# Optimization experiments

Measured on AMD Instinct MI355X. Metric: run time of the kernel, lower is better.

## Reference

```python
import jax, jax.numpy as jnp
import numpy as np

LAYERS, STACKS = 10, 4
DILATIONS = [2 ** l for _ in range(STACKS) for l in range(LAYERS)]  # 40 blocks


def setup_inputs() -> dict:
    key = jax.random.key(0)
    ks = jax.random.split(key, 7)
    B, C, L, SC, NB = 4, 64, 8192, 256, len(DILATIONS)
    scale = 0.05  # keep 40 stacked residual blocks numerically tame
    return {
        "x": jax.random.normal(ks[0], (B, C, L), dtype=jnp.float32),
        "dc_w": jax.random.normal(ks[1], (NB, C, C, 2), dtype=jnp.float32) * scale,
        "dc_b": jax.random.normal(ks[2], (NB, C), dtype=jnp.float32) * scale,
        "conv_w": jax.random.normal(ks[3], (NB, C, C), dtype=jnp.float32) * scale,
        "conv_b": jax.random.normal(ks[4], (NB, C), dtype=jnp.float32) * scale,
        "skip_w": jax.random.normal(ks[5], (NB, SC, C), dtype=jnp.float32) * scale,
        "skip_b": jax.random.normal(ks[6], (NB, SC), dtype=jnp.float32) * scale,
        "skip_size": 4096,
    }


def reference(x, dc_w, dc_b, conv_w, conv_b, skip_w, skip_b, skip_size):
    # x: [B, res_ch, L]; returns stacked skips [n_blocks, B, skip_ch, skip_size]
    out = x
    skips = []
    for i, d in enumerate(DILATIONS):
        h = (jnp.einsum('oi,bil->bol', dc_w[i, :, :, 0], out[:, :, :-d])
             + jnp.einsum('oi,bil->bol', dc_w[i, :, :, 1], out[:, :, d:])
             + dc_b[i][None, :, None])
        g = jax.nn.relu(h)
        r = jnp.einsum('oi,bil->bol', conv_w[i], g) + conv_b[i][None, :, None]
        out = r + out[:, :, -r.shape[2]:]  # residual on aligned (last) timesteps
        s = jnp.einsum('oi,bil->bol', skip_w[i], g) + skip_b[i][None, :, None]
        skips.append(s[:, :, -skip_size:])
    return jnp.stack(skips)
```

## Files before the change

### kernel.cpp

```cpp
#include <hip/hip_runtime.h>


#define CC    64
#define SCC   256
#define BB    4
#define LL0   8192
#define NBLK  40
#define SKIPN 4096

typedef __attribute__((ext_vector_type(8))) short bf16x8;
typedef __attribute__((ext_vector_type(4))) float f32x4;
typedef unsigned short us;

__device__ __forceinline__ us f2bf(float f) {
    union { float f; unsigned u; } v; v.f = f;
    return (us)((v.u + 0x7FFF + ((v.u >> 16) & 1)) >> 16);
}
__device__ __forceinline__ unsigned pk2(float a, float b) {
    return (unsigned)f2bf(a) | ((unsigned)f2bf(b) << 16);
}
__device__ __forceinline__ uint2 pk4(f32x4 v) {
    return (uint2){pk2(v[0], v[1]), pk2(v[2], v[3])};
}
__device__ __forceinline__ bf16x8 pack8(f32x4 u0, f32x4 u1) {
    bf16x8 r;
    r[0]=(short)f2bf(u0[0]); r[1]=(short)f2bf(u0[1]);
    r[2]=(short)f2bf(u0[2]); r[3]=(short)f2bf(u0[3]);
    r[4]=(short)f2bf(u1[0]); r[5]=(short)f2bf(u1[1]);
    r[6]=(short)f2bf(u1[2]); r[7]=(short)f2bf(u1[3]);
    return r;
}
__device__ __forceinline__ int sws(int r, int c) {
    return (r << 6) + ((((c >> 3) ^ r) & 7) << 3) + (c & 7);
}
__device__ __forceinline__ int scb(int s, int chunk) {
    return (s << 6) + (((chunk ^ (s & 7)) & 7) << 3);
}

__global__ __launch_bounds__(256) void prep_kernel(
    const float* __restrict__ x, float* __restrict__ xt_out,
    const float* __restrict__ dc_w, const float* __restrict__ conv_w,
    const float* __restrict__ skip_w,
    us* __restrict__ wcat, us* __restrict__ cwb, us* __restrict__ swb)
{
    if (blockIdx.x < 512) {
        __shared__ float tile[64][65];
        const int b = blockIdx.x >> 7, t0 = (blockIdx.x & 127) * 64;
        const int tid = threadIdx.x;
        #pragma unroll
        for (int p = 0; p < 4; ++p) {
            const int c = p * 16 + (tid >> 4), j = tid & 15;
            const float4 v = *(const float4*)(x + ((size_t)b * CC + c) * LL0 + t0 + j * 4);
            tile[c][j*4+0]=v.x; tile[c][j*4+1]=v.y; tile[c][j*4+2]=v.z; tile[c][j*4+3]=v.w;
        }
        __syncthreads();
        #pragma unroll
        for (int p = 0; p < 4; ++p) {
            const int r = p * 16 + (tid >> 4), h = tid & 15;
            float4 v = {tile[h*4+0][r], tile[h*4+1][r], tile[h*4+2][r], tile[h*4+3][r]};
            *(float4*)(xt_out + ((size_t)b * LL0 + t0 + r) * CC + h * 4) = v;
        }
        return;
    }
    const int n_sw = NBLK * SCC * CC, n_cw = NBLK * CC * CC, n_wc = NBLK * CC * 128;
    for (int idx = (blockIdx.x - 512) * blockDim.x + threadIdx.x; idx < n_sw;
         idx += 1024 * blockDim.x) {
        swb[idx] = f2bf(skip_w[idx]);
        if (idx < n_cw) cwb[idx] = f2bf(conv_w[idx]);
        if (idx < n_wc) {
            const int i = idx >> 13, o = (idx >> 7) & 63, kk = idx & 127;
            wcat[idx] = f2bf(dc_w[(((i * CC + o) * CC) + (kk & 63)) * 2 + (kk >> 6)]);
        }
    }
}

template<int NW>
__device__ __forceinline__ void skip_body(
    int e, int blk0,
    const us* __restrict__ g_all, const us* __restrict__ swb,
    const float* __restrict__ skip_b, float* __restrict__ out)
{
    constexpr int ROWS = NW * 16;
    constexpr int TPB = (SKIPN / ROWS) * BB;
    const int tid = threadIdx.x, lane = tid & 63, wv = tid >> 6;
    const int j = blk0 + e / TPB;
    const int id = e % TPB;
    const int tt = id % (SKIPN / ROWS);
    const int b  = id / (SKIPN / ROWS);
    const us* g  = g_all + ((size_t)j * BB + b) * SKIPN * CC;
    const us* sw = swb + (size_t)j * SCC * CC;
    const float* sb = skip_b + j * SCC;
    float* op = out + ((size_t)j * BB + b) * SCC * SKIPN;

    const int trow = tt * ROWS + wv * 16 + (lane & 15);
    bf16x8 a[2];
    a[0] = *(const bf16x8*)(g + (size_t)trow * CC + (lane >> 4) * 8);
    a[1] = *(const bf16x8*)(g + (size_t)trow * CC + 32 + (lane >> 4) * 8);
    const int tstore = tt * ROWS + wv * 16 + ((lane >> 4) << 2);
    #pragma unroll 4
    for (int n = 0; n < 16; ++n) {
        const int sc = n * 16 + (lane & 15);
        const float bias = sb[sc];
        f32x4 acc = (f32x4){bias, bias, bias, bias};
        const us* wrow = sw + sc * CC + (lane >> 4) * 8;
        acc = __builtin_amdgcn_mfma_f32_16x16x32_bf16(a[0], *(const bf16x8*)(wrow), acc, 0, 0, 0);
        acc = __builtin_amdgcn_mfma_f32_16x16x32_bf16(a[1], *(const bf16x8*)(wrow + 32), acc, 0, 0, 0);
        *(float4*)(op + (size_t)sc * SKIPN + tstore) = (float4){acc[0], acc[1], acc[2], acc[3]};
    }
}

__global__ __launch_bounds__(512) void fused6_kernel(
    const float* __restrict__ cur, float* __restrict__ nxt,
    const us* __restrict__ wcat_all, const us* __restrict__ cwb_all,
    const float* __restrict__ db_all, const float* __restrict__ cb_all,
    us* __restrict__ g_all, int blk0, int Lin, int ntiles,
    const us* __restrict__ swb, const float* __restrict__ skip_b,
    float* __restrict__ out, int pb0)
{
    const int wg = blockIdx.x, chain = BB * ntiles;
    if (wg >= chain) { skip_body<8>(wg - chain, pb0, g_all, swb, skip_b, out); return; }

    constexpr int TOUT = 96, R0 = 159, RCAP = 160;
    __shared__ __align__(16) float sm[RCAP * CC];
    __shared__ __align__(16) us  scr[8 * 16 * CC];

    const int tid = threadIdx.x, lane = tid & 63, wv = tid >> 6;
    const int b = wg / ntiles, t0 = (wg % ntiles) * TOUT;
    const float* src = cur + (size_t)b * LL0 * CC;
    const int s = lane & 15, q = lane >> 4;
    us* myscr = scr + wv * (16 * CC);

    for (int base = 0; base < R0; base += 32) {
        const int row = base + (tid >> 4);
        const int h4 = (tid & 15) * 4;
        if (row < R0) {
            int gt = t0 + row; if (gt > Lin - 1) gt = Lin - 1;
            *(f32x4*)(sm + sws(row, h4)) = *(const f32x4*)(src + (size_t)gt * CC + h4);
        }
    }
    __syncthreads();

    int Rcur = R0, Lj = Lin;
    for (int j = 0; j < 6; ++j) {
        const int d = 1 << j;
        const int Rn = Rcur - d;
        Lj -= d;
        const us* wj = wcat_all + (size_t)(blk0 + j) * CC * 128;
        const us* cj = cwb_all + (size_t)(blk0 + j) * CC * CC;
        const float* dbj = db_all + (blk0 + j) * CC;
        const float* cbj = cb_all + (blk0 + j) * CC;
        const int wbase = Lj - SKIPN;
        us* gdst = g_all + ((size_t)(blk0 + j) * BB + b) * SKIPN * CC;

        f32x4 r2[2][4];
        #pragma unroll
        for (int fi = 0; fi < 2; ++fi) {
            const int fg = wv + fi * 8;
            const bool act = fg * 16 < Rn;
            if (act) {
                const int t = fg * 16 + s;
                const int tc = t > Rn - 1 ? Rn - 1 : t;
                bf16x8 af0 = pack8(*(const f32x4*)(sm + sws(tc, q * 8)),
                                   *(const f32x4*)(sm + sws(tc, q * 8 + 4)));
                bf16x8 af1 = pack8(*(const f32x4*)(sm + sws(tc, 32 + q * 8)),
                                   *(const f32x4*)(sm + sws(tc, 36 + q * 8)));
                bf16x8 af2 = pack8(*(const f32x4*)(sm + sws(tc + d, q * 8)),
                                   *(const f32x4*)(sm + sws(tc + d, q * 8 + 4)));
                bf16x8 af3 = pack8(*(const f32x4*)(sm + sws(tc + d, 32 + q * 8)),
                                   *(const f32x4*)(sm + sws(tc + d, 36 + q * 8)));
                #pragma unroll
                for (int n = 0; n < 4; ++n) {
                    const int o0 = n * 16 + q * 4;
                    f32x4 acc = *(const f32x4*)(dbj + o0);
                    const us* wr = wj + (n * 16 + s) * 128 + q * 8;
                    acc = __builtin_amdgcn_mfma_f32_16x16x32_bf16(*(const bf16x8*)(wr),      af0, acc, 0, 0, 0);
                    acc = __builtin_amdgcn_mfma_f32_16x16x32_bf16(*(const bf16x8*)(wr + 32), af1, acc, 0, 0, 0);
                    acc = __builtin_amdgcn_mfma_f32_16x16x32_bf16(*(const bf16x8*)(wr + 64), af2, acc, 0, 0, 0);
                    acc = __builtin_amdgcn_mfma_f32_16x16x32_bf16(*(const bf16x8*)(wr + 96), af3, acc, 0, 0, 0);
                    #pragma unroll
                    for (int r = 0; r < 4; ++r) acc[r] = acc[r] > 0.f ? acc[r] : 0.f;
                    *(uint2*)(myscr + scb(s, n * 2 + (q >> 1)) + (q & 1) * 4) = pk4(acc);
                }
                {
                    const int gt = t0 + t;
                    if (t < Rn && gt >= wbase && gt < Lj) {
                        us* gr = gdst + (size_t)(gt - wbase) * CC;
                        #pragma unroll
                        for (int h = 0; h < 2; ++h) {
                            const int ck = q * 2 + h;
                            *(bf16x8*)(gr + ck * 8) = *(const bf16x8*)(myscr + scb(s, ck));
                        }
                    }
                }
                bf16x8 g0 = *(const bf16x8*)(myscr + scb(s, q));
                bf16x8 g1 = *(const bf16x8*)(myscr + scb(s, 4 + q));
                #pragma unroll
                for (int n = 0; n < 4; ++n) {
                    const int o0 = n * 16 + q * 4;
                    f32x4 r = *(const f32x4*)(cbj + o0);
                    const us* wr = cj + (n * 16 + s) * CC + q * 8;
                    r = __builtin_amdgcn_mfma_f32_16x16x32_bf16(*(const bf16x8*)(wr),      g0, r, 0, 0, 0);
                    r = __builtin_amdgcn_mfma_f32_16x16x32_bf16(*(const bf16x8*)(wr + 32), g1, r, 0, 0, 0);
                    r += *(const f32x4*)(sm + sws(tc + d, o0));
                    r2[fi][n] = r;
                }
            }
        }
        __syncthreads();
        #pragma unroll
        for (int fi = 0; fi < 2; ++fi) {
            const int fg = wv + fi * 8;
            const int t = fg * 16 + s;
            if (t < Rn) {
                #pragma unroll
                for (int n = 0; n < 4; ++n)
                    *(f32x4*)(sm + sws(t, n * 16 + q * 4)) = r2[fi][n];
            }
        }
        __syncthreads();
        Rcur = Rn;
    }

    float* dst = nxt + (size_t)b * LL0 * CC;
    for (int base = 0; base < TOUT; base += 32) {
        const int row = base + (tid >> 4);
        const int h4 = (tid & 15) * 4;
        const int gt = t0 + row;
        if (row < TOUT && gt < Lj)
            *(float4*)(dst + (size_t)gt * CC + h4) = *(const float4*)(sm + sws(row, h4));
    }
}

template<int D>
__global__ __launch_bounds__(256) void pair_kernel(
    const float* __restrict__ cur, float* __restrict__ nxt,
    const us* __restrict__ wA, const us* __restrict__ wB,
    const us* __restrict__ cA, const us* __restrict__ cB,
    const float* __restrict__ dbA, const float* __restrict__ dbB,
    const float* __restrict__ cbA, const float* __restrict__ cbB,
    us* __restrict__ gA_out, us* __restrict__ gB_out,
    int Lin, int ntB,
    const us* __restrict__ g_all, const us* __restrict__ swb,
    const float* __restrict__ skip_b, float* __restrict__ out, int pb0)
{
    const int wg = blockIdx.x, chain = BB * ntB;
    if (wg >= chain) { skip_body<4>(wg - chain, pb0, g_all, swb, skip_b, out); return; }

    __shared__ __align__(16) float xs[4 * 32 * CC];
    __shared__ __align__(16) float ms[2 * 32 * CC];
    __shared__ __align__(16) us  scr[4 * 16 * CC];

    const int tid = threadIdx.x, lane = tid & 63, wv = tid >> 6;
    const int b = wg / ntB, T0 = (wg % ntB) * 32;
    const float* src = cur + (size_t)b * LL0 * CC;
    const int s = lane & 15, q = lane >> 4;
    us* myscr = scr + wv * (16 * CC);
    const int LoutA = Lin - D, Lout2 = Lin - 3 * D;

    #pragma unroll
    for (int p = 0; p < 8; ++p) {
        const int row = p * 16 + (tid >> 4);
        const int st = row >> 5, r = row & 31;
        const int h4 = (tid & 15) * 4;
        int gt = T0 + st * D + r; if (gt > Lin - 1) gt = Lin - 1;
        *(f32x4*)(xs + st * (32 * CC) + sws(r, h4)) =
            *(const f32x4*)(src + (size_t)gt * CC + h4);
    }
    __syncthreads();

    {
        const int m = wv >> 1, rA = (wv & 1) * 16 + s;
        const int tA = T0 + m * 2 * D + rA;
        const float* x0 = xs + (2 * m) * (32 * CC);
        const float* x1 = xs + (2 * m + 1) * (32 * CC);
        bf16x8 af0 = pack8(*(const f32x4*)(x0 + sws(rA, q * 8)),
                           *(const f32x4*)(x0 + sws(rA, q * 8 + 4)));
        bf16x8 af1 = pack8(*(const f32x4*)(x0 + sws(rA, 32 + q * 8)),
                           *(const f32x4*)(x0 + sws(rA, 36 + q * 8)));
        bf16x8 af2 = pack8(*(const f32x4*)(x1 + sws(rA, q * 8)),
                           *(const f32x4*)(x1 + sws(rA, q * 8 + 4)));
        bf16x8 af3 = pack8(*(const f32x4*)(x1 + sws(rA, 32 + q * 8)),
                           *(const f32x4*)(x1 + sws(rA, 36 + q * 8)));
        #pragma unroll
        for (int n = 0; n < 4; ++n) {
            const int o0 = n * 16 + q * 4;
            f32x4 acc = *(const f32x4*)(dbA + o0);
            const us* wr = wA + (n * 16 + s) * 128 + q * 8;
            acc = __builtin_amdgcn_mfma_f32_16x16x32_bf16(*(const bf16x8*)(wr),      af0, acc, 0, 0, 0);
            acc = __builtin_amdgcn_mfma_f32_16x16x32_bf16(*(const bf16x8*)(wr + 32), af1, acc, 0, 0, 0);
            acc = __builtin_amdgcn_mfma_f32_16x16x32_bf16(*(const bf16x8*)(wr + 64), af2, acc, 0, 0, 0);
            acc = __builtin_amdgcn_mfma_f32_16x16x32_bf16(*(const bf16x8*)(wr + 96), af3, acc, 0, 0, 0);
            #pragma unroll
            for (int r = 0; r < 4; ++r) acc[r] = acc[r] > 0.f ? acc[r] : 0.f;
            *(uint2*)(myscr + scb(s, n * 2 + (q >> 1)) + (q & 1) * 4) = pk4(acc);
        }
        {
            const int wbA = LoutA - SKIPN;
            const bool own = (m == 0) || (tA >= ntB * 32);
            if (own && tA >= wbA && tA < LoutA) {
                us* gr = gA_out + ((size_t)b * SKIPN + (tA - wbA)) * CC;
                #pragma unroll
                for (int h = 0; h < 2; ++h) {
                    const int ck = q * 2 + h;
                    *(bf16x8*)(gr + ck * 8) = *(const bf16x8*)(myscr + scb(s, ck));
                }
            }
        }
        bf16x8 g0 = *(const bf16x8*)(myscr + scb(s, q));
        bf16x8 g1 = *(const bf16x8*)(myscr + scb(s, 4 + q));
        #pragma unroll
        for (int n = 0; n < 4; ++n) {
            const int o0 = n * 16 + q * 4;
            f32x4 r = *(const f32x4*)(cbA + o0);
            const us* wr = cA + (n * 16 + s) * CC + q * 8;
            r = __builtin_amdgcn_mfma_f32_16x16x32_bf16(*(const bf16x8*)(wr),      g0, r, 0, 0, 0);
            r = __builtin_amdgcn_mfma_f32_16x16x32_bf16(*(const bf16x8*)(wr + 32), g1, r, 0, 0, 0);
            r += *(const f32x4*)(x1 + sws(rA, o0));
            *(f32x4*)(ms + m * (32 * CC) + sws(rA, o0)) = r;
        }
    }
    __syncthreads();

    {
        const int rB = (wv & 1) * 16 + s;
        const int tB = T0 + rB;
        const bool lead = wv < 2;
        const float* m0 = ms;
        const float* m1 = ms + 32 * CC;
        bf16x8 af0 = pack8(*(const f32x4*)(m0 + sws(rB, q * 8)),
                           *(const f32x4*)(m0 + sws(rB, q * 8 + 4)));
        bf16x8 af1 = pack8(*(const f32x4*)(m0 + sws(rB, 32 + q * 8)),
                           *(const f32x4*)(m0 + sws(rB, 36 + q * 8)));
        bf16x8 af2 = pack8(*(const f32x4*)(m1 + sws(rB, q * 8)),
                           *(const f32x4*)(m1 + sws(rB, q * 8 + 4)));
        bf16x8 af3 = pack8(*(const f32x4*)(m1 + sws(rB, 32 + q * 8)),
                           *(const f32x4*)(m1 + sws(rB, 36 + q * 8)));
        #pragma unroll
        for (int n = 0; n < 4; ++n) {
            const int o0 = n * 16 + q * 4;
            f32x4 acc = *(const f32x4*)(dbB + o0);
            const us* wr = wB + (n * 16 + s) * 128 + q * 8;
            acc = __builtin_amdgcn_mfma_f32_16x16x32_bf16(*(const bf16x8*)(wr),      af0, acc, 0, 0, 0);
            acc = __builtin_amdgcn_mfma_f32_16x16x32_bf16(*(const bf16x8*)(wr + 32), af1, acc, 0, 0, 0);
            acc = __builtin_amdgcn_mfma_f32_16x16x32_bf16(*(const bf16x8*)(wr + 64), af2, acc, 0, 0, 0);
            acc = __builtin_amdgcn_mfma_f32_16x16x32_bf16(*(const bf16x8*)(wr + 96), af3, acc, 0, 0, 0);
            #pragma unroll
            for (int r = 0; r < 4; ++r) acc[r] = acc[r] > 0.f ? acc[r] : 0.f;
            *(uint2*)(myscr + scb(s, n * 2 + (q >> 1)) + (q & 1) * 4) = pk4(acc);
        }
        {
            const int wbB = Lout2 - SKIPN;
            if (lead && tB >= wbB && tB < Lout2) {
                us* gr = gB_out + ((size_t)b * SKIPN + (tB - wbB)) * CC;
                #pragma unroll
                for (int h = 0; h < 2; ++h) {
                    const int ck = q * 2 + h;
                    *(bf16x8*)(gr + ck * 8) = *(const bf16x8*)(myscr + scb(s, ck));
                }
            }
        }
        bf16x8 g0 = *(const bf16x8*)(myscr + scb(s, q));
        bf16x8 g1 = *(const bf16x8*)(myscr + scb(s, 4 + q));
        float* dst = nxt + (size_t)b * LL0 * CC;
        #pragma unroll
        for (int n = 0; n < 4; ++n) {
            const int o0 = n * 16 + q * 4;
            f32x4 r = *(const f32x4*)(cbB + o0);
            const us* wr = cB + (n * 16 + s) * CC + q * 8;
            r = __builtin_amdgcn_mfma_f32_16x16x32_bf16(*(const bf16x8*)(wr),      g0, r, 0, 0, 0);
            r = __builtin_amdgcn_mfma_f32_16x16x32_bf16(*(const bf16x8*)(wr + 32), g1, r, 0, 0, 0);
            r += *(const f32x4*)(m1 + sws(rB, o0));
            if (lead && tB < Lout2)
                *(f32x4*)(dst + (size_t)tB * CC + o0) = r;
        }
    }
}

__global__ __launch_bounds__(256) void skip_kernel(
    const us* __restrict__ g_all, const us* __restrict__ swb,
    const float* __restrict__ skip_b, float* __restrict__ out, int blk0)
{
    skip_body<4>(blockIdx.x, blk0, g_all, swb, skip_b, out);
}

extern "C" void kernel_launch(void* const* d_in, const int* in_sizes, int n_in,
                              void* d_out, int out_size, void* d_ws, size_t ws_size,
                              hipStream_t stream)
{
    const float* x      = (const float*)d_in[0];
    const float* dc_w   = (const float*)d_in[1];
    const float* dc_b   = (const float*)d_in[2];
    const float* conv_w = (const float*)d_in[3];
    const float* conv_b = (const float*)d_in[4];
    const float* skip_w = (const float*)d_in[5];
    const float* skip_b = (const float*)d_in[6];
    float* out = (float*)d_out;

    char* ws = (char*)d_ws;
    float* bufA = (float*)ws;  ws += (size_t)BB * LL0 * CC * 4;
    float* bufB = (float*)ws;  ws += (size_t)BB * LL0 * CC * 4;
    us* g_all = (us*)ws;       ws += (size_t)NBLK * BB * SKIPN * CC * 2;
    us* wcat  = (us*)ws;       ws += (size_t)NBLK * CC * 128 * 2;
    us* cwb   = (us*)ws;       ws += (size_t)NBLK * CC * CC * 2;
    us* swb   = (us*)ws;       ws += (size_t)NBLK * SCC * CC * 2;

    prep_kernel<<<1536, 256, 0, stream>>>(x, bufA, dc_w, conv_w, skip_w, wcat, cwb, swb);

    float* bufs[2] = {bufA, bufB};
    const size_t GSZ = (size_t)BB * SKIPN * CC;
    int Lc = LL0, blk = 0, q = 0, produced = 0, skipped = 0;
    for (int st = 0; st < 4; ++st) {
        {
            const int Lout = Lc - 63;
            const int nt = (Lout + 95) / 96;
            int cap = produced - skipped; if (cap > 4) cap = 4;
            fused6_kernel<<<dim3(BB * nt + cap * 128), 512, 0, stream>>>(
                bufs[q & 1], bufs[(q + 1) & 1], wcat, cwb, dc_b, conv_b,
                g_all, blk, Lc, nt, swb, skip_b, out, skipped);
            skipped += cap; produced += 6; blk += 6; Lc = Lout; ++q;
        }
        #pragma unroll
        for (int pi = 0; pi < 2; ++pi) {
            const int D = pi == 0 ? 64 : 256;
            const int Lout2 = Lc - 3 * D;
            const int nt = (Lout2 + 31) / 32;
            int cap = produced - skipped; if (cap > 4) cap = 4;
            const int grid = BB * nt + cap * 256;
            if (D == 64)
                pair_kernel<64><<<dim3(grid), 256, 0, stream>>>(
                    bufs[q & 1], bufs[(q + 1) & 1],
                    wcat + (size_t)blk * CC * 128, wcat + (size_t)(blk + 1) * CC * 128,
                    cwb + (size_t)blk * CC * CC, cwb + (size_t)(blk + 1) * CC * CC,
                    dc_b + blk * CC, dc_b + (blk + 1) * CC,
                    conv_b + blk * CC, conv_b + (blk + 1) * CC,
                    g_all + (size_t)blk * GSZ, g_all + (size_t)(blk + 1) * GSZ,
                    Lc, nt, g_all, swb, skip_b, out, skipped);
            else
                pair_kernel<256><<<dim3(grid), 256, 0, stream>>>(
                    bufs[q & 1], bufs[(q + 1) & 1],
                    wcat + (size_t)blk * CC * 128, wcat + (size_t)(blk + 1) * CC * 128,
                    cwb + (size_t)blk * CC * CC, cwb + (size_t)(blk + 1) * CC * CC,
                    dc_b + blk * CC, dc_b + (blk + 1) * CC,
                    conv_b + blk * CC, conv_b + (blk + 1) * CC,
                    g_all + (size_t)blk * GSZ, g_all + (size_t)(blk + 1) * GSZ,
                    Lc, nt, g_all, swb, skip_b, out, skipped);
            skipped += cap; produced += 2; blk += 2; Lc = Lout2; ++q;
        }
    }
    const int rem = NBLK - skipped;
    if (rem > 0)
        skip_kernel<<<dim3(rem * 256), 256, 0, stream>>>(g_all, swb, skip_b, out, skipped);
}
```

Measured before the change: 770.5 us.

## Move skip GEMMs into one final kernel and keep bf16 shadow copy in fused6

Skip-projection work is no longer piggybacked as extra workgroups inside the fused6 and pair chain kernels. All 40 blocks' skip outputs are now computed by a single skip_all_kernel launched at the end. Separately, fused6 keeps a bf16 copy of the residual tile in shared memory, so the MFMA A-operands are loaded directly instead of being converted from fp32 on every read. This gives up the overlap of skip writes with the sequential chain and adds shared memory and extra stores in exchange for less conversion work and simpler chain kernels.

```diff
diff --git a/kernel.cpp b/kernel.cpp
--- a/kernel.cpp
+++ b/kernel.cpp
@@ -22,15 +22,10 @@
 __device__ __forceinline__ uint2 pk4(f32x4 v) {
     return (uint2){pk2(v[0], v[1]), pk2(v[2], v[3])};
 }
-__device__ __forceinline__ bf16x8 pack8(f32x4 u0, f32x4 u1) {
-    bf16x8 r;
-    r[0]=(short)f2bf(u0[0]); r[1]=(short)f2bf(u0[1]);
-    r[2]=(short)f2bf(u0[2]); r[3]=(short)f2bf(u0[3]);
-    r[4]=(short)f2bf(u1[0]); r[5]=(short)f2bf(u1[1]);
-    r[6]=(short)f2bf(u1[2]); r[7]=(short)f2bf(u1[3]);
-    return r;
-}
 __device__ __forceinline__ int sws(int r, int c) {
+    return (r << 6) + ((((c >> 3) ^ r) & 7) << 3) + (c & 7);
+}
+__device__ __forceinline__ int swh(int r, int c) {
     return (r << 6) + ((((c >> 3) ^ r) & 7) << 3) + (c & 7);
 }
 __device__ __forceinline__ int scb(int s, int chunk) {
@@ -74,58 +69,19 @@
     }
 }
 
-template<int NW>
-__device__ __forceinline__ void skip_body(
-    int e, int blk0,
-    const us* __restrict__ g_all, const us* __restrict__ swb,
-    const float* __restrict__ skip_b, float* __restrict__ out)
-{
-    constexpr int ROWS = NW * 16;
-    constexpr int TPB = (SKIPN / ROWS) * BB;
-    const int tid = threadIdx.x, lane = tid & 63, wv = tid >> 6;
-    const int j = blk0 + e / TPB;
-    const int id = e % TPB;
-    const int tt = id % (SKIPN / ROWS);
-    const int b  = id / (SKIPN / ROWS);
-    const us* g  = g_all + ((size_t)j * BB + b) * SKIPN * CC;
-    const us* sw = swb + (size_t)j * SCC * CC;
-    const float* sb = skip_b + j * SCC;
-    float* op = out + ((size_t)j * BB + b) * SCC * SKIPN;
-
-    const int trow = tt * ROWS + wv * 16 + (lane & 15);
-    bf16x8 a[2];
-    a[0] = *(const bf16x8*)(g + (size_t)trow * CC + (lane >> 4) * 8);
-    a[1] = *(const bf16x8*)(g + (size_t)trow * CC + 32 + (lane >> 4) * 8);
-    const int tstore = tt * ROWS + wv * 16 + ((lane >> 4) << 2);
-    #pragma unroll 4
-    for (int n = 0; n < 16; ++n) {
-        const int sc = n * 16 + (lane & 15);
-        const float bias = sb[sc];
-        f32x4 acc = (f32x4){bias, bias, bias, bias};
-        const us* wrow = sw + sc * CC + (lane >> 4) * 8;
-        acc = __builtin_amdgcn_mfma_f32_16x16x32_bf16(a[0], *(const bf16x8*)(wrow), acc, 0, 0, 0);
-        acc = __builtin_amdgcn_mfma_f32_16x16x32_bf16(a[1], *(const bf16x8*)(wrow + 32), acc, 0, 0, 0);
-        *(float4*)(op + (size_t)sc * SKIPN + tstore) = (float4){acc[0], acc[1], acc[2], acc[3]};
-    }
-}
-
 __global__ __launch_bounds__(512) void fused6_kernel(
     const float* __restrict__ cur, float* __restrict__ nxt,
     const us* __restrict__ wcat_all, const us* __restrict__ cwb_all,
     const float* __restrict__ db_all, const float* __restrict__ cb_all,
-    us* __restrict__ g_all, int blk0, int Lin, int ntiles,
-    const us* __restrict__ swb, const float* __restrict__ skip_b,
-    float* __restrict__ out, int pb0)
+    us* __restrict__ g_all, int blk0, int Lin, int ntiles)
 {
-    const int wg = blockIdx.x, chain = BB * ntiles;
-    if (wg >= chain) { skip_body<8>(wg - chain, pb0, g_all, swb, skip_b, out); return; }
-
     constexpr int TOUT = 96, R0 = 159, RCAP = 160;
     __shared__ __align__(16) float sm[RCAP * CC];
+    __shared__ __align__(16) us  smb[RCAP * CC];
     __shared__ __align__(16) us  scr[8 * 16 * CC];
 
     const int tid = threadIdx.x, lane = tid & 63, wv = tid >> 6;
-    const int b = wg / ntiles, t0 = (wg % ntiles) * TOUT;
+    const int b = blockIdx.x / ntiles, t0 = (blockIdx.x % ntiles) * TOUT;
     const float* src = cur + (size_t)b * LL0 * CC;
     const int s = lane & 15, q = lane >> 4;
     us* myscr = scr + wv * (16 * CC);
@@ -135,7 +91,9 @@
         const int h4 = (tid & 15) * 4;
         if (row < R0) {
             int gt = t0 + row; if (gt > Lin - 1) gt = Lin - 1;
-            *(f32x4*)(sm + sws(row, h4)) = *(const f32x4*)(src + (size_t)gt * CC + h4);
+            f32x4 v = *(const f32x4*)(src + (size_t)gt * CC + h4);
+            *(f32x4*)(sm + sws(row, h4)) = v;
+            *(uint2*)(smb + swh(row, h4)) = pk4(v);
         }
     }
     __syncthreads();
@@ -156,18 +114,13 @@
         #pragma unroll
         for (int fi = 0; fi < 2; ++fi) {
             const int fg = wv + fi * 8;
-            const bool act = fg * 16 < Rn;
-            if (act) {
+            if (fg * 16 < Rn) {
                 const int t = fg * 16 + s;
                 const int tc = t > Rn - 1 ? Rn - 1 : t;
-                bf16x8 af0 = pack8(*(const f32x4*)(sm + sws(tc, q * 8)),
-                                   *(const f32x4*)(sm + sws(tc, q * 8 + 4)));
-                bf16x8 af1 = pack8(*(const f32x4*)(sm + sws(tc, 32 + q * 8)),
-                                   *(const f32x4*)(sm + sws(tc, 36 + q * 8)));
-                bf16x8 af2 = pack8(*(const f32x4*)(sm + sws(tc + d, q * 8)),
-                                   *(const f32x4*)(sm + sws(tc + d, q * 8 + 4)));
-                bf16x8 af3 = pack8(*(const f32x4*)(sm + sws(tc + d, 32 + q * 8)),
-                                   *(const f32x4*)(sm + sws(tc + d, 36 + q * 8)));
+                bf16x8 af0 = *(const bf16x8*)(smb + swh(tc,     q * 8));
+                bf16x8 af1 = *(const bf16x8*)(smb + swh(tc,     32 + q * 8));
+                bf16x8 af2 = *(const bf16x8*)(smb + swh(tc + d, q * 8));
+                bf16x8 af3 = *(const bf16x8*)(smb + swh(tc + d, 32 + q * 8));
                 #pragma unroll
                 for (int n = 0; n < 4; ++n) {
                     const int o0 = n * 16 + q * 4;
@@ -181,6 +134,8 @@
                     for (int r = 0; r < 4; ++r) acc[r] = acc[r] > 0.f ? acc[r] : 0.f;
                     *(uint2*)(myscr + scb(s, n * 2 + (q >> 1)) + (q & 1) * 4) = pk4(acc);
                 }
+                bf16x8 g0 = *(const bf16x8*)(myscr + scb(s, q));
+                bf16x8 g1 = *(const bf16x8*)(myscr + scb(s, 4 + q));
                 {
                     const int gt = t0 + t;
                     if (t < Rn && gt >= wbase && gt < Lj) {
@@ -192,8 +147,6 @@
                         }
                     }
                 }
-                bf16x8 g0 = *(const bf16x8*)(myscr + scb(s, q));
-                bf16x8 g1 = *(const bf16x8*)(myscr + scb(s, 4 + q));
                 #pragma unroll
                 for (int n = 0; n < 4; ++n) {
                     const int o0 = n * 16 + q * 4;
@@ -213,8 +166,11 @@
             const int t = fg * 16 + s;
             if (t < Rn) {
                 #pragma unroll
-                for (int n = 0; n < 4; ++n)
-                    *(f32x4*)(sm + sws(t, n * 16 + q * 4)) = r2[fi][n];
+                for (int n = 0; n < 4; ++n) {
+                    const int o0 = n * 16 + q * 4;
+                    *(f32x4*)(sm + sws(t, o0)) = r2[fi][n];
+                    *(uint2*)(smb + swh(t, o0)) = pk4(r2[fi][n]);
+                }
             }
         }
         __syncthreads();
@@ -239,19 +195,14 @@
     const float* __restrict__ dbA, const float* __restrict__ dbB,
     const float* __restrict__ cbA, const float* __restrict__ cbB,
     us* __restrict__ gA_out, us* __restrict__ gB_out,
-    int Lin, int ntB,
-    const us* __restrict__ g_all, const us* __restrict__ swb,
-    const float* __restrict__ skip_b, float* __restrict__ out, int pb0)
+    int Lin, int ntB)
 {
-    const int wg = blockIdx.x, chain = BB * ntB;
-    if (wg >= chain) { skip_body<4>(wg - chain, pb0, g_all, swb, skip_b, out); return; }
-
     __shared__ __align__(16) float xs[4 * 32 * CC];
     __shared__ __align__(16) float ms[2 * 32 * CC];
     __shared__ __align__(16) us  scr[4 * 16 * CC];
 
     const int tid = threadIdx.x, lane = tid & 63, wv = tid >> 6;
-    const int b = wg / ntB, T0 = (wg % ntB) * 32;
+    const int b = blockIdx.x / ntB, T0 = (blockIdx.x % ntB) * 32;
     const float* src = cur + (size_t)b * LL0 * CC;
     const int s = lane & 15, q = lane >> 4;
     us* myscr = scr + wv * (16 * CC);
@@ -273,14 +224,25 @@
         const int tA = T0 + m * 2 * D + rA;
         const float* x0 = xs + (2 * m) * (32 * CC);
         const float* x1 = xs + (2 * m + 1) * (32 * CC);
-        bf16x8 af0 = pack8(*(const f32x4*)(x0 + sws(rA, q * 8)),
-                           *(const f32x4*)(x0 + sws(rA, q * 8 + 4)));
-        bf16x8 af1 = pack8(*(const f32x4*)(x0 + sws(rA, 32 + q * 8)),
-                           *(const f32x4*)(x0 + sws(rA, 36 + q * 8)));
-        bf16x8 af2 = pack8(*(const f32x4*)(x1 + sws(rA, q * 8)),
-                           *(const f32x4*)(x1 + sws(rA, q * 8 + 4)));
-        bf16x8 af3 = pack8(*(const f32x4*)(x1 + sws(rA, 32 + q * 8)),
-                           *(const f32x4*)(x1 + sws(rA, 36 + q * 8)));
+        bf16x8 af0, af1, af2, af3;
+        {
+            f32x4 a = *(const f32x4*)(x0 + sws(rA, q * 8));
+            f32x4 bb = *(const f32x4*)(x0 + sws(rA, q * 8 + 4));
+            af0 = (bf16x8){(short)f2bf(a[0]),(short)f2bf(a[1]),(short)f2bf(a[2]),(short)f2bf(a[3]),
+                           (short)f2bf(bb[0]),(short)f2bf(bb[1]),(short)f2bf(bb[2]),(short)f2bf(bb[3])};
+            a = *(const f32x4*)(x0 + sws(rA, 32 + q * 8));
+            bb = *(const f32x4*)(x0 + sws(rA, 36 + q * 8));
+            af1 = (bf16x8){(short)f2bf(a[0]),(short)f2bf(a[1]),(short)f2bf(a[2]),(short)f2bf(a[3]),
+                           (short)f2bf(bb[0]),(short)f2bf(bb[1]),(short)f2bf(bb[2]),(short)f2bf(bb[3])};
+            a = *(const f32x4*)(x1 + sws(rA, q * 8));
+            bb = *(const f32x4*)(x1 + sws(rA, q * 8 + 4));
+            af2 = (bf16x8){(short)f2bf(a[0]),(short)f2bf(a[1]),(short)f2bf(a[2]),(short)f2bf(a[3]),
+                           (short)f2bf(bb[0]),(short)f2bf(bb[1]),(short)f2bf(bb[2]),(short)f2bf(bb[3])};
+            a = *(const f32x4*)(x1 + sws(rA, 32 + q * 8));
+            bb = *(const f32x4*)(x1 + sws(rA, 36 + q * 8));
+            af3 = (bf16x8){(short)f2bf(a[0]),(short)f2bf(a[1]),(short)f2bf(a[2]),(short)f2bf(a[3]),
+                           (short)f2bf(bb[0]),(short)f2bf(bb[1]),(short)f2bf(bb[2]),(short)f2bf(bb[3])};
+        }
         #pragma unroll
         for (int n = 0; n < 4; ++n) {
             const int o0 = n * 16 + q * 4;
@@ -327,14 +289,25 @@
         const bool lead = wv < 2;
         const float* m0 = ms;
         const float* m1 = ms + 32 * CC;
-        bf16x8 af0 = pack8(*(const f32x4*)(m0 + sws(rB, q * 8)),
-                           *(const f32x4*)(m0 + sws(rB, q * 8 + 4)));
-        bf16x8 af1 = pack8(*(const f32x4*)(m0 + sws(rB, 32 + q * 8)),
-                           *(const f32x4*)(m0 + sws(rB, 36 + q * 8)));
-        bf16x8 af2 = pack8(*(const f32x4*)(m1 + sws(rB, q * 8)),
-                           *(const f32x4*)(m1 + sws(rB, q * 8 + 4)));
-        bf16x8 af3 = pack8(*(const f32x4*)(m1 + sws(rB, 32 + q * 8)),
-                           *(const f32x4*)(m1 + sws(rB, 36 + q * 8)));
+        bf16x8 af0, af1, af2, af3;
+        {
+            f32x4 a = *(const f32x4*)(m0 + sws(rB, q * 8));
+            f32x4 bb = *(const f32x4*)(m0 + sws(rB, q * 8 + 4));
+            af0 = (bf16x8){(short)f2bf(a[0]),(short)f2bf(a[1]),(short)f2bf(a[2]),(short)f2bf(a[3]),
+                           (short)f2bf(bb[0]),(short)f2bf(bb[1]),(short)f2bf(bb[2]),(short)f2bf(bb[3])};
+            a = *(const f32x4*)(m0 + sws(rB, 32 + q * 8));
+            bb = *(const f32x4*)(m0 + sws(rB, 36 + q * 8));
+            af1 = (bf16x8){(short)f2bf(a[0]),(short)f2bf(a[1]),(short)f2bf(a[2]),(short)f2bf(a[3]),
+                           (short)f2bf(bb[0]),(short)f2bf(bb[1]),(short)f2bf(bb[2]),(short)f2bf(bb[3])};
+            a = *(const f32x4*)(m1 + sws(rB, q * 8));
+            bb = *(const f32x4*)(m1 + sws(rB, q * 8 + 4));
+            af2 = (bf16x8){(short)f2bf(a[0]),(short)f2bf(a[1]),(short)f2bf(a[2]),(short)f2bf(a[3]),
+                           (short)f2bf(bb[0]),(short)f2bf(bb[1]),(short)f2bf(bb[2]),(short)f2bf(bb[3])};
+            a = *(const f32x4*)(m1 + sws(rB, 32 + q * 8));
+            bb = *(const f32x4*)(m1 + sws(rB, 36 + q * 8));
+            af3 = (bf16x8){(short)f2bf(a[0]),(short)f2bf(a[1]),(short)f2bf(a[2]),(short)f2bf(a[3]),
+                           (short)f2bf(bb[0]),(short)f2bf(bb[1]),(short)f2bf(bb[2]),(short)f2bf(bb[3])};
+        }
         #pragma unroll
         for (int n = 0; n < 4; ++n) {
             const int o0 = n * 16 + q * 4;
@@ -376,11 +349,38 @@
     }
 }
 
-__global__ __launch_bounds__(256) void skip_kernel(
+__global__ __launch_bounds__(256) void skip_all_kernel(
     const us* __restrict__ g_all, const us* __restrict__ swb,
-    const float* __restrict__ skip_b, float* __restrict__ out, int blk0)
+    const float* __restrict__ skip_b, float* __restrict__ out)
 {
-    skip_body<4>(blockIdx.x, blk0, g_all, swb, skip_b, out);
+    const int ntile = SKIPN / 64;
+    const int tid = threadIdx.x, lane = tid & 63, wv = tid >> 6;
+    int id = blockIdx.x;
+    const int tt = id % ntile; id /= ntile;
+    const int b  = id % BB;    id /= BB;
+    const int blk = id;
+
+    const us* g  = g_all + ((size_t)blk * BB + b) * SKIPN * CC;
+    const us* sw = swb + (size_t)blk * SCC * CC;
+    const float* sb = skip_b + blk * SCC;
+    float* op = out + ((size_t)blk * BB + b) * SCC * SKIPN;
+
+    const int trow = tt * 64 + wv * 16 + (lane & 15);
+    bf16x8 a[2];
+    a[0] = *(const bf16x8*)(g + (size_t)trow * CC + (lane >> 4) * 8);
+    a[1] = *(const bf16x8*)(g + (size_t)trow * CC + 32 + (lane >> 4) * 8);
+
+    const int tstore = tt * 64 + wv * 16 + ((lane >> 4) << 2);
+    #pragma unroll 4
+    for (int n = 0; n < 16; ++n) {
+        const int sc = n * 16 + (lane & 15);
+        const float bias = sb[sc];
+        f32x4 acc = (f32x4){bias, bias, bias, bias};
+        const us* wrow = sw + sc * CC + (lane >> 4) * 8;
+        acc = __builtin_amdgcn_mfma_f32_16x16x32_bf16(a[0], *(const bf16x8*)(wrow), acc, 0, 0, 0);
+        acc = __builtin_amdgcn_mfma_f32_16x16x32_bf16(a[1], *(const bf16x8*)(wrow + 32), acc, 0, 0, 0);
+        *(float4*)(op + (size_t)sc * SKIPN + tstore) = (float4){acc[0], acc[1], acc[2], acc[3]};
+    }
 }
 
 extern "C" void kernel_launch(void* const* d_in, const int* in_sizes, int n_in,
@@ -400,54 +400,50 @@
     float* bufA = (float*)ws;  ws += (size_t)BB * LL0 * CC * 4;
     float* bufB = (float*)ws;  ws += (size_t)BB * LL0 * CC * 4;
     us* g_all = (us*)ws;       ws += (size_t)NBLK * BB * SKIPN * CC * 2;
-    us* wcat  = (us*)ws;       ws += (size_t)NBLK * CC * 128 * 2;
-    us* cwb   = (us*)ws;       ws += (size_t)NBLK * CC * CC * 2;
-    us* swb   = (us*)ws;       ws += (size_t)NBLK * SCC * CC * 2;
+    us* wcat = (us*)ws;        ws += (size_t)NBLK * CC * 128 * 2;
+    us* cwb  = (us*)ws;        ws += (size_t)NBLK * CC * CC * 2;
+    us* swb  = (us*)ws;        ws += (size_t)NBLK * SCC * CC * 2;
 
     prep_kernel<<<1536, 256, 0, stream>>>(x, bufA, dc_w, conv_w, skip_w, wcat, cwb, swb);
 
     float* bufs[2] = {bufA, bufB};
     const size_t GSZ = (size_t)BB * SKIPN * CC;
-    int Lc = LL0, blk = 0, q = 0, produced = 0, skipped = 0;
+    int Lc = LL0, blk = 0, qq = 0;
     for (int st = 0; st < 4; ++st) {
         {
             const int Lout = Lc - 63;
             const int nt = (Lout + 95) / 96;
-            int cap = produced - skipped; if (cap > 4) cap = 4;
-            fused6_kernel<<<dim3(BB * nt + cap * 128), 512, 0, stream>>>(
-                bufs[q & 1], bufs[(q + 1) & 1], wcat, cwb, dc_b, conv_b,
-                g_all, blk, Lc, nt, swb, skip_b, out, skipped);
-            skipped += cap; produced += 6; blk += 6; Lc = Lout; ++q;
-        }
-        #pragma unroll
+            fused6_kernel<<<dim3(BB * nt), 512, 0, stream>>>(
+                bufs[qq & 1], bufs[(qq + 1) & 1], wcat, cwb, dc_b, conv_b,
+                g_all, blk, Lc, nt);
+            blk += 6; Lc = Lout; ++qq;
+        }
         for (int pi = 0; pi < 2; ++pi) {
             const int D = pi == 0 ? 64 : 256;
             const int Lout2 = Lc - 3 * D;
             const int nt = (Lout2 + 31) / 32;
-            int cap = produced - skipped; if (cap > 4) cap = 4;
-            const int grid = BB * nt + cap * 256;
             if (D == 64)
-                pair_kernel<64><<<dim3(grid), 256, 0, stream>>>(
-                    bufs[q & 1], bufs[(q + 1) & 1],
+                pair_kernel<64><<<dim3(BB * nt), 256, 0, stream>>>(
+                    bufs[qq & 1], bufs[(qq + 1) & 1],
                     wcat + (size_t)blk * CC * 128, wcat + (size_t)(blk + 1) * CC * 128,
                     cwb + (size_t)blk * CC * CC, cwb + (size_t)(blk + 1) * CC * CC,
                     dc_b + blk * CC, dc_b + (blk + 1) * CC,
                     conv_b + blk * CC, conv_b + (blk + 1) * CC,
                     g_all + (size_t)blk * GSZ, g_all + (size_t)(blk + 1) * GSZ,
-                    Lc, nt, g_all, swb, skip_b, out, skipped);
+                    Lc, nt);
             else
-                pair_kernel<256><<<dim3(grid), 256, 0, stream>>>(
-                    bufs[q & 1], bufs[(q + 1) & 1],
+                pair_kernel<256><<<dim3(BB * nt), 256, 0, stream>>>(
+                    bufs[qq & 1], bufs[(qq + 1) & 1],
                     wcat + (size_t)blk * CC * 128, wcat + (size_t)(blk + 1) * CC * 128,
                     cwb + (size_t)blk * CC * CC, cwb + (size_t)(blk + 1) * CC * CC,
                     dc_b + blk * CC, dc_b + (blk + 1) * CC,
                     conv_b + blk * CC, conv_b + (blk + 1) * CC,
                     g_all + (size_t)blk * GSZ, g_all + (size_t)(blk + 1) * GSZ,
-                    Lc, nt, g_all, swb, skip_b, out, skipped);
-            skipped += cap; produced += 2; blk += 2; Lc = Lout2; ++q;
-        }
-    }
-    const int rem = NBLK - skipped;
-    if (rem > 0)
-        skip_kernel<<<dim3(rem * 256), 256, 0, stream>>>(g_all, swb, skip_b, out, skipped);
-}
+                    Lc, nt);
+            blk += 2; Lc = Lout2; ++qq;
+        }
+    }
+
+    skip_all_kernel<<<dim3(NBLK * BB * (SKIPN / 64)), 256, 0, stream>>>(
+        g_all, swb, skip_b, out);
+}
```

Result: slower. 834.6 us (+8.3%).

## Keep bf16 shadow copies of activations in LDS and rebalance skip work

Applied to the files above, without the earlier changes.

The fused6 kernel now keeps a bf16 copy of the residual tile in shared memory alongside the fp32 copy. MFMA operands load directly from it instead of converting eight floats each time. The pair kernel stores inputs and intermediates only as bf16, loads the fp32 residual straight from global memory into registers, and keeps fp32 only for the middle residual. The caps on how many skip blocks each launch absorbs are rebalanced so fused6 takes fewer and the pair kernels take more. The trade is extra LDS footprint and conversion work at store time, in exchange for fewer repeated conversions and less LDS read traffic.

```diff
diff --git a/kernel.cpp b/kernel.cpp
--- a/kernel.cpp
+++ b/kernel.cpp
@@ -22,15 +22,10 @@
 __device__ __forceinline__ uint2 pk4(f32x4 v) {
     return (uint2){pk2(v[0], v[1]), pk2(v[2], v[3])};
 }
-__device__ __forceinline__ bf16x8 pack8(f32x4 u0, f32x4 u1) {
-    bf16x8 r;
-    r[0]=(short)f2bf(u0[0]); r[1]=(short)f2bf(u0[1]);
-    r[2]=(short)f2bf(u0[2]); r[3]=(short)f2bf(u0[3]);
-    r[4]=(short)f2bf(u1[0]); r[5]=(short)f2bf(u1[1]);
-    r[6]=(short)f2bf(u1[2]); r[7]=(short)f2bf(u1[3]);
-    return r;
-}
 __device__ __forceinline__ int sws(int r, int c) {
+    return (r << 6) + ((((c >> 3) ^ r) & 7) << 3) + (c & 7);
+}
+__device__ __forceinline__ int swh(int r, int c) {
     return (r << 6) + ((((c >> 3) ^ r) & 7) << 3) + (c & 7);
 }
 __device__ __forceinline__ int scb(int s, int chunk) {
@@ -122,6 +117,7 @@
 
     constexpr int TOUT = 96, R0 = 159, RCAP = 160;
     __shared__ __align__(16) float sm[RCAP * CC];
+    __shared__ __align__(16) us  smb[RCAP * CC];
     __shared__ __align__(16) us  scr[8 * 16 * CC];
 
     const int tid = threadIdx.x, lane = tid & 63, wv = tid >> 6;
@@ -135,7 +131,9 @@
         const int h4 = (tid & 15) * 4;
         if (row < R0) {
             int gt = t0 + row; if (gt > Lin - 1) gt = Lin - 1;
-            *(f32x4*)(sm + sws(row, h4)) = *(const f32x4*)(src + (size_t)gt * CC + h4);
+            f32x4 v = *(const f32x4*)(src + (size_t)gt * CC + h4);
+            *(f32x4*)(sm + sws(row, h4)) = v;
+            *(uint2*)(smb + swh(row, h4)) = pk4(v);
         }
     }
     __syncthreads();
@@ -156,18 +154,13 @@
         #pragma unroll
         for (int fi = 0; fi < 2; ++fi) {
             const int fg = wv + fi * 8;
-            const bool act = fg * 16 < Rn;
-            if (act) {
+            if (fg * 16 < Rn) {
                 const int t = fg * 16 + s;
                 const int tc = t > Rn - 1 ? Rn - 1 : t;
-                bf16x8 af0 = pack8(*(const f32x4*)(sm + sws(tc, q * 8)),
-                                   *(const f32x4*)(sm + sws(tc, q * 8 + 4)));
-                bf16x8 af1 = pack8(*(const f32x4*)(sm + sws(tc, 32 + q * 8)),
-                                   *(const f32x4*)(sm + sws(tc, 36 + q * 8)));
-                bf16x8 af2 = pack8(*(const f32x4*)(sm + sws(tc + d, q * 8)),
-                                   *(const f32x4*)(sm + sws(tc + d, q * 8 + 4)));
-                bf16x8 af3 = pack8(*(const f32x4*)(sm + sws(tc + d, 32 + q * 8)),
-                                   *(const f32x4*)(sm + sws(tc + d, 36 + q * 8)));
+                bf16x8 af0 = *(const bf16x8*)(smb + swh(tc,     q * 8));
+                bf16x8 af1 = *(const bf16x8*)(smb + swh(tc,     32 + q * 8));
+                bf16x8 af2 = *(const bf16x8*)(smb + swh(tc + d, q * 8));
+                bf16x8 af3 = *(const bf16x8*)(smb + swh(tc + d, 32 + q * 8));
                 #pragma unroll
                 for (int n = 0; n < 4; ++n) {
                     const int o0 = n * 16 + q * 4;
@@ -181,6 +174,8 @@
                     for (int r = 0; r < 4; ++r) acc[r] = acc[r] > 0.f ? acc[r] : 0.f;
                     *(uint2*)(myscr + scb(s, n * 2 + (q >> 1)) + (q & 1) * 4) = pk4(acc);
                 }
+                bf16x8 g0 = *(const bf16x8*)(myscr + scb(s, q));
+                bf16x8 g1 = *(const bf16x8*)(myscr + scb(s, 4 + q));
                 {
                     const int gt = t0 + t;
                     if (t < Rn && gt >= wbase && gt < Lj) {
@@ -192,8 +187,6 @@
                         }
                     }
                 }
-                bf16x8 g0 = *(const bf16x8*)(myscr + scb(s, q));
-                bf16x8 g1 = *(const bf16x8*)(myscr + scb(s, 4 + q));
                 #pragma unroll
                 for (int n = 0; n < 4; ++n) {
                     const int o0 = n * 16 + q * 4;
@@ -213,8 +206,11 @@
             const int t = fg * 16 + s;
             if (t < Rn) {
                 #pragma unroll
-                for (int n = 0; n < 4; ++n)
-                    *(f32x4*)(sm + sws(t, n * 16 + q * 4)) = r2[fi][n];
+                for (int n = 0; n < 4; ++n) {
+                    const int o0 = n * 16 + q * 4;
+                    *(f32x4*)(sm + sws(t, o0)) = r2[fi][n];
+                    *(uint2*)(smb + swh(t, o0)) = pk4(r2[fi][n]);
+                }
             }
         }
         __syncthreads();
@@ -246,9 +242,10 @@
     const int wg = blockIdx.x, chain = BB * ntB;
     if (wg >= chain) { skip_body<4>(wg - chain, pb0, g_all, swb, skip_b, out); return; }
 
-    __shared__ __align__(16) float xs[4 * 32 * CC];
-    __shared__ __align__(16) float ms[2 * 32 * CC];
-    __shared__ __align__(16) us  scr[4 * 16 * CC];
+    __shared__ __align__(16) us   xsb[4 * 32 * CC];
+    __shared__ __align__(16) us   msb[2 * 32 * CC];
+    __shared__ __align__(16) float mf[32 * CC];
+    __shared__ __align__(16) us   scr[4 * 16 * CC];
 
     const int tid = threadIdx.x, lane = tid & 63, wv = tid >> 6;
     const int b = wg / ntB, T0 = (wg % ntB) * 32;
@@ -263,24 +260,28 @@
         const int st = row >> 5, r = row & 31;
         const int h4 = (tid & 15) * 4;
         int gt = T0 + st * D + r; if (gt > Lin - 1) gt = Lin - 1;
-        *(f32x4*)(xs + st * (32 * CC) + sws(r, h4)) =
-            *(const f32x4*)(src + (size_t)gt * CC + h4);
+        f32x4 v = *(const f32x4*)(src + (size_t)gt * CC + h4);
+        *(uint2*)(xsb + st * (32 * CC) + swh(r, h4)) = pk4(v);
+    }
+
+    const int mA = wv >> 1, rA = (wv & 1) * 16 + s;
+    const int tA = T0 + mA * 2 * D + rA;
+    f32x4 resA[4];
+    {
+        int tr = tA + D; if (tr > Lin - 1) tr = Lin - 1;
+        #pragma unroll
+        for (int n = 0; n < 4; ++n)
+            resA[n] = *(const f32x4*)(src + (size_t)tr * CC + n * 16 + q * 4);
     }
     __syncthreads();
 
     {
-        const int m = wv >> 1, rA = (wv & 1) * 16 + s;
-        const int tA = T0 + m * 2 * D + rA;
-        const float* x0 = xs + (2 * m) * (32 * CC);
-        const float* x1 = xs + (2 * m + 1) * (32 * CC);
-        bf16x8 af0 = pack8(*(const f32x4*)(x0 + sws(rA, q * 8)),
-                           *(const f32x4*)(x0 + sws(rA, q * 8 + 4)));
-        bf16x8 af1 = pack8(*(const f32x4*)(x0 + sws(rA, 32 + q * 8)),
-                           *(const f32x4*)(x0 + sws(rA, 36 + q * 8)));
-        bf16x8 af2 = pack8(*(const f32x4*)(x1 + sws(rA, q * 8)),
-                           *(const f32x4*)(x1 + sws(rA, q * 8 + 4)));
-        bf16x8 af3 = pack8(*(const f32x4*)(x1 + sws(rA, 32 + q * 8)),
-                           *(const f32x4*)(x1 + sws(rA, 36 + q * 8)));
+        const us* x0b = xsb + (2 * mA) * (32 * CC);
+        const us* x1b = xsb + (2 * mA + 1) * (32 * CC);
+        bf16x8 af0 = *(const bf16x8*)(x0b + swh(rA, q * 8));
+        bf16x8 af1 = *(const bf16x8*)(x0b + swh(rA, 32 + q * 8));
+        bf16x8 af2 = *(const bf16x8*)(x1b + swh(rA, q * 8));
+        bf16x8 af3 = *(const bf16x8*)(x1b + swh(rA, 32 + q * 8));
         #pragma unroll
         for (int n = 0; n < 4; ++n) {
             const int o0 = n * 16 + q * 4;
@@ -296,7 +297,7 @@
         }
         {
             const int wbA = LoutA - SKIPN;
-            const bool own = (m == 0) || (tA >= ntB * 32);
+            const bool own = (mA == 0) || (tA >= ntB * 32);
             if (own && tA >= wbA && tA < LoutA) {
                 us* gr = gA_out + ((size_t)b * SKIPN + (tA - wbA)) * CC;
                 #pragma unroll
@@ -315,8 +316,9 @@
             const us* wr = cA + (n * 16 + s) * CC + q * 8;
             r = __builtin_amdgcn_mfma_f32_16x16x32_bf16(*(const bf16x8*)(wr),      g0, r, 0, 0, 0);
             r = __builtin_amdgcn_mfma_f32_16x16x32_bf16(*(const bf16x8*)(wr + 32), g1, r, 0, 0, 0);
-            r += *(const f32x4*)(x1 + sws(rA, o0));
-            *(f32x4*)(ms + m * (32 * CC) + sws(rA, o0)) = r;
+            r += resA[n];
+            *(uint2*)(msb + mA * (32 * CC) + swh(rA, o0)) = pk4(r);
+            if (mA == 1) *(f32x4*)(mf + sws(rA, o0)) = r;
         }
     }
     __syncthreads();
@@ -325,16 +327,10 @@
         const int rB = (wv & 1) * 16 + s;
         const int tB = T0 + rB;
         const bool lead = wv < 2;
-        const float* m0 = ms;
-        const float* m1 = ms + 32 * CC;
-        bf16x8 af0 = pack8(*(const f32x4*)(m0 + sws(rB, q * 8)),
-                           *(const f32x4*)(m0 + sws(rB, q * 8 + 4)));
-        bf16x8 af1 = pack8(*(const f32x4*)(m0 + sws(rB, 32 + q * 8)),
-                           *(const f32x4*)(m0 + sws(rB, 36 + q * 8)));
-        bf16x8 af2 = pack8(*(const f32x4*)(m1 + sws(rB, q * 8)),
-                           *(const f32x4*)(m1 + sws(rB, q * 8 + 4)));
-        bf16x8 af3 = pack8(*(const f32x4*)(m1 + sws(rB, 32 + q * 8)),
-                           *(const f32x4*)(m1 + sws(rB, 36 + q * 8)));
+        bf16x8 af0 = *(const bf16x8*)(msb + swh(rB, q * 8));
+        bf16x8 af1 = *(const bf16x8*)(msb + swh(rB, 32 + q * 8));
+        bf16x8 af2 = *(const bf16x8*)(msb + (32 * CC) + swh(rB, q * 8));
+        bf16x8 af3 = *(const bf16x8*)(msb + (32 * CC) + swh(rB, 32 + q * 8));
         #pragma unroll
         for (int n = 0; n < 4; ++n) {
             const int o0 = n * 16 + q * 4;
@@ -369,7 +365,7 @@
             const us* wr = cB + (n * 16 + s) * CC + q * 8;
             r = __builtin_amdgcn_mfma_f32_16x16x32_bf16(*(const bf16x8*)(wr),      g0, r, 0, 0, 0);
             r = __builtin_amdgcn_mfma_f32_16x16x32_bf16(*(const bf16x8*)(wr + 32), g1, r, 0, 0, 0);
-            r += *(const f32x4*)(m1 + sws(rB, o0));
+            r += *(const f32x4*)(mf + sws(rB, o0));
             if (lead && tB < Lout2)
                 *(f32x4*)(dst + (size_t)tB * CC + o0) = r;
         }
@@ -400,35 +396,34 @@
     float* bufA = (float*)ws;  ws += (size_t)BB * LL0 * CC * 4;
     float* bufB = (float*)ws;  ws += (size_t)BB * LL0 * CC * 4;
     us* g_all = (us*)ws;       ws += (size_t)NBLK * BB * SKIPN * CC * 2;
-    us* wcat  = (us*)ws;       ws += (size_t)NBLK * CC * 128 * 2;
-    us* cwb   = (us*)ws;       ws += (size_t)NBLK * CC * CC * 2;
-    us* swb   = (us*)ws;       ws += (size_t)NBLK * SCC * CC * 2;
+    us* wcat = (us*)ws;        ws += (size_t)NBLK * CC * 128 * 2;
+    us* cwb  = (us*)ws;        ws += (size_t)NBLK * CC * CC * 2;
+    us* swb  = (us*)ws;        ws += (size_t)NBLK * SCC * CC * 2;
 
     prep_kernel<<<1536, 256, 0, stream>>>(x, bufA, dc_w, conv_w, skip_w, wcat, cwb, swb);
 
     float* bufs[2] = {bufA, bufB};
     const size_t GSZ = (size_t)BB * SKIPN * CC;
-    int Lc = LL0, blk = 0, q = 0, produced = 0, skipped = 0;
+    int Lc = LL0, blk = 0, qq = 0, produced = 0, skipped = 0;
     for (int st = 0; st < 4; ++st) {
         {
             const int Lout = Lc - 63;
             const int nt = (Lout + 95) / 96;
-            int cap = produced - skipped; if (cap > 4) cap = 4;
+            int cap = produced - skipped; if (cap > 1) cap = 1;
             fused6_kernel<<<dim3(BB * nt + cap * 128), 512, 0, stream>>>(
-                bufs[q & 1], bufs[(q + 1) & 1], wcat, cwb, dc_b, conv_b,
+                bufs[qq & 1], bufs[(qq + 1) & 1], wcat, cwb, dc_b, conv_b,
                 g_all, blk, Lc, nt, swb, skip_b, out, skipped);
-            skipped += cap; produced += 6; blk += 6; Lc = Lout; ++q;
-        }
-        #pragma unroll
+            skipped += cap; produced += 6; blk += 6; Lc = Lout; ++qq;
+        }
         for (int pi = 0; pi < 2; ++pi) {
             const int D = pi == 0 ? 64 : 256;
             const int Lout2 = Lc - 3 * D;
             const int nt = (Lout2 + 31) / 32;
-            int cap = produced - skipped; if (cap > 4) cap = 4;
+            int cap = produced - skipped; if (cap > 5) cap = 5;
             const int grid = BB * nt + cap * 256;
             if (D == 64)
                 pair_kernel<64><<<dim3(grid), 256, 0, stream>>>(
-                    bufs[q & 1], bufs[(q + 1) & 1],
+                    bufs[qq & 1], bufs[(qq + 1) & 1],
                     wcat + (size_t)blk * CC * 128, wcat + (size_t)(blk + 1) * CC * 128,
                     cwb + (size_t)blk * CC * CC, cwb + (size_t)(blk + 1) * CC * CC,
                     dc_b + blk * CC, dc_b + (blk + 1) * CC,
@@ -437,14 +432,14 @@
                     Lc, nt, g_all, swb, skip_b, out, skipped);
             else
                 pair_kernel<256><<<dim3(grid), 256, 0, stream>>>(
-                    bufs[q & 1], bufs[(q + 1) & 1],
+                    bufs[qq & 1], bufs[(qq + 1) & 1],
                     wcat + (size_t)blk * CC * 128, wcat + (size_t)(blk + 1) * CC * 128,
                     cwb + (size_t)blk * CC * CC, cwb + (size_t)(blk + 1) * CC * CC,
                     dc_b + blk * CC, dc_b + (blk + 1) * CC,
                     conv_b + blk * CC, conv_b + (blk + 1) * CC,
                     g_all + (size_t)blk * GSZ, g_all + (size_t)(blk + 1) * GSZ,
                     Lc, nt, g_all, swb, skip_b, out, skipped);
-            skipped += cap; produced += 2; blk += 2; Lc = Lout2; ++q;
+            skipped += cap; produced += 2; blk += 2; Lc = Lout2; ++qq;
         }
     }
     const int rem = NBLK - skipped;
```

Measured after the change: 776.1 us. About the same (+0.7%).
